# Performance work log

Hardware: AMD Instinct MI355X
Metric: run time of the kernel (lower is better)

Reference implementation:

```python
import jax, jax.numpy as jnp
import numpy as np

N = 20000      # total nodes (20 proteins x 1000 residues)
E = 320000     # edges (avg degree 16)
F_IN = 22      # amino-acid feature dim
H = 4          # attention heads
C = 64         # hidden dim per head
HC = H * C     # 256
G = 20         # number of graphs
OUT = 128      # output embedding dim
NEG_SLOPE = 0.2


def setup_inputs() -> dict:
    key = jax.random.key(0)
    ks = jax.random.split(key, 24)
    x = jax.random.normal(ks[0], (N, F_IN), dtype=jnp.float32)
    edge_index = jax.random.randint(ks[1], (2, E), 0, N)
    batch = jnp.arange(N, dtype=jnp.int64) // (N // G)  # 1000 nodes per graph
    s = 0.1
    d = {
        'x': x, 'edge_index': edge_index, 'batch': batch,
        'Win': jax.random.normal(ks[2], (F_IN, C)) * s,
        'bin_': jnp.zeros((C,), jnp.float32),
        'Wout': jax.random.normal(ks[3], (2 * HC, OUT)) * s,
        'bout': jnp.zeros((OUT,), jnp.float32),
    }
    kidx = 4
    for i in range(3):
        in_dim = C if i == 0 else HC
        d[f'Wl{i}'] = jax.random.normal(ks[kidx], (in_dim, HC)) * s; kidx += 1
        d[f'Wr{i}'] = jax.random.normal(ks[kidx], (in_dim, HC)) * s; kidx += 1
        d[f'att{i}'] = jax.random.normal(ks[kidx], (H, C)) * s; kidx += 1
        d[f'b{i}'] = jnp.zeros((HC,), jnp.float32)
    return d


def _gatv2_layer(h, src, dst, Wl, Wr, att, bias):
    # PyG GATv2Conv (share_weights=False, concat=True), dropout off (eval)
    xl = (h @ Wl).reshape(-1, H, C)   # source transform (x_j)
    xr = (h @ Wr).reshape(-1, H, C)   # target transform (x_i)
    e = jax.nn.leaky_relu(xl[src] + xr[dst], NEG_SLOPE)  # [E+N, H, C]
    logit = jnp.einsum('ehc,hc->eh', e, att)             # [E+N, H]
    mx = jax.ops.segment_max(logit, dst, num_segments=N)
    mx = jnp.where(jnp.isfinite(mx), mx, 0.0)
    ex = jnp.exp(logit - mx[dst])
    den = jax.ops.segment_sum(ex, dst, num_segments=N)
    alpha = ex / (den[dst] + 1e-16)                      # segment softmax
    out = jax.ops.segment_sum(alpha[:, :, None] * xl[src], dst, num_segments=N)
    return out.reshape(-1, HC) + bias


def reference(x, edge_index, batch, Win, bin_,
              Wl0, Wr0, att0, b0, Wl1, Wr1, att1, b1, Wl2, Wr2, att2, b2,
              Wout, bout):
    # add self-loops once (add_self_loops=True in every GATv2Conv)
    loops = jnp.arange(N, dtype=edge_index.dtype)
    src = jnp.concatenate([edge_index[0], loops])
    dst = jnp.concatenate([edge_index[1], loops])

    h = jax.nn.relu(x @ Win + bin_)  # input_proj + ReLU (dropout = eval identity)
    layers = [(Wl0, Wr0, att0, b0), (Wl1, Wr1, att1, b1), (Wl2, Wr2, att2, b2)]
    for (Wl, Wr, att, b) in layers:
        h_prev = h
        h = jax.nn.elu(_gatv2_layer(h, src, dst, Wl, Wr, att, b))
        if h_prev.shape[-1] == h.shape[-1]:  # residual when dims match (layers 1,2)
            h = h + h_prev

    counts = jax.ops.segment_sum(jnp.ones((N,), h.dtype), batch, num_segments=G)
    x_mean = jax.ops.segment_sum(h, batch, num_segments=G) / counts[:, None]
    x_max = jax.ops.segment_max(h, batch, num_segments=G)
    x_global = jnp.concatenate([x_mean, x_max], axis=-1)  # [G, 512]
    return x_global @ Wout + bout                          # [G, 128]
```

## Files before the change

kernel.cpp:

```cpp
#include <hip/hip_runtime.h>
#include <hip/hip_bf16.h>
#include <math.h>

#define N_NODES 20000
#define N_EDGES 320000
#define F_IN 22
#define H_HEADS 4
#define C_DIM 64
#define HC 256
#define G_GRAPHS 20
#define OUT_DIM 128
#define NODES_PER_G 1000
#define POOL_CHUNKS 8
#define NODES_PER_CHUNK (NODES_PER_G / POOL_CHUNKS)
#define ELL_CAP 64
#define SCAT_NB ((N_EDGES + 255) / 256)
#define INPROJ_NB (N_NODES / 4)

#if __has_builtin(__builtin_amdgcn_exp2f)
#define EXP2F __builtin_amdgcn_exp2f
#else
#define EXP2F exp2f
#endif

typedef unsigned short ushortT;
typedef __attribute__((ext_vector_type(8))) short short8;
typedef __attribute__((ext_vector_type(4))) float v4f;
typedef __attribute__((ext_vector_type(2))) float f2;

typedef const __attribute__((address_space(1))) void* gas_p;
typedef __attribute__((address_space(3))) void* las_p;

__device__ inline ushortT f2bf(float f) {
    unsigned int u = __float_as_uint(f);
    unsigned int r = (u + 0x7fffu + ((u >> 16) & 1u)) >> 16;
    return (ushortT)r;
}

__global__ __launch_bounds__(256) void front_kernel(
        const int* __restrict__ esrc, const int* __restrict__ edst,
        int* __restrict__ fill, int* __restrict__ ell,
        const float* __restrict__ x, const float* __restrict__ Win,
        const float* __restrict__ bin, ushortT* __restrict__ h0b,
        const float* __restrict__ Wl0, const float* __restrict__ Wr0,
        const float* __restrict__ Wl1, const float* __restrict__ Wr1,
        const float* __restrict__ Wl2, const float* __restrict__ Wr2,
        ushortT* __restrict__ Bt0, ushortT* __restrict__ Bt1, ushortT* __restrict__ Bt2) {
    int tid = threadIdx.x;
    if (blockIdx.x < SCAT_NB) {
        int i = blockIdx.x * 256 + tid;
        if (i < N_EDGES) {
            int d = edst[i];
            int p = atomicAdd(&fill[d], 1);
            if (p < ELL_CAP) ell[(d << 6) + p] = esrc[i];
        }
        return;
    }
    if (blockIdx.x < SCAT_NB + INPROJ_NB) {
        int node = (blockIdx.x - SCAT_NB) * 4 + (tid >> 6);
        int c = tid & 63;
        float acc = bin[c];
        const float* xr = x + node * F_IN;
#pragma unroll
        for (int f = 0; f < F_IN; f++) acc += xr[f] * Win[f * C_DIM + c];
        h0b[node * C_DIM + c] = f2bf(acc > 0.f ? acc : 0.f);
        return;
    }
    int flat = blockIdx.x - SCAT_NB - INPROJ_NB;
    int z = flat >> 6;
    int rem = flat & 63;
    int kx = (rem >> 3) * 32;
    int nx = (rem & 7) * 32;
    int layer = z >> 1, isR = z & 1;
    const float* src; ushortT* dst; int K;
    if (layer == 0)      { K = 64;  dst = Bt0; src = isR ? Wr0 : Wl0; }
    else if (layer == 1) { K = 256; dst = Bt1; src = isR ? Wr1 : Wl1; }
    else                 { K = 256; dst = Bt2; src = isR ? Wr2 : Wl2; }
    if (kx >= K) return;
    __shared__ float tile[32][33];
    int c = tid & 31, r8 = tid >> 5;
#pragma unroll
    for (int i = 0; i < 4; i++) {
        int kk = r8 + i * 8;
        tile[kk][c] = src[(kx + kk) * 256 + nx + c];
    }
    __syncthreads();
    int nbase = isR ? 256 : 0;
#pragma unroll
    for (int i = 0; i < 4; i++) {
        int nn = r8 + i * 8;
        dst[(size_t)(nbase + nx + nn) * K + kx + c] = f2bf(tile[c][nn]);
    }
}

#define GBM 128
#define GBN 128
#define GBK 32

__global__ __launch_bounds__(256) void gemm_mfma_kernel(
        const ushortT* __restrict__ A, const ushortT* __restrict__ Bt,
        ushortT* __restrict__ XLb, ushortT* __restrict__ XRb, int M, int K) {
    __shared__ ushortT As[GBM * GBK];
    __shared__ ushortT Bs[GBN * GBK];
    int tid = threadIdx.x;
    int wave = tid >> 6, lane = tid & 63;
    int wm = wave & 1, wn = wave >> 1;
    int bm0 = blockIdx.y * GBM;
    int bn0 = blockIdx.x * GBN;

    v4f acc[4][4];
#pragma unroll
    for (int mt = 0; mt < 4; mt++)
#pragma unroll
        for (int nt = 0; nt < 4; nt++) acc[mt][nt] = (v4f){0.f, 0.f, 0.f, 0.f};

    int srow = lane >> 2;
    int scol = (lane & 3) * 8;
    int arow0 = wave * 16 + srow;
    int arow1 = arow0 + 64;
    int ag0 = bm0 + arow0; if (ag0 >= M) ag0 = 0;
    int ag1 = bm0 + arow1; if (ag1 >= M) ag1 = 0;
    const ushortT* aptr0 = A + (size_t)ag0 * K + scol;
    const ushortT* aptr1 = A + (size_t)ag1 * K + scol;
    const ushortT* bptr0 = Bt + (size_t)(bn0 + arow0) * K + scol;
    const ushortT* bptr1 = Bt + (size_t)(bn0 + arow1) * K + scol;
    las_p lA0 = (las_p)&As[(wave * 16) * GBK];
    las_p lA1 = (las_p)&As[(wave * 16 + 64) * GBK];
    las_p lB0 = (las_p)&Bs[(wave * 16) * GBK];
    las_p lB1 = (las_p)&Bs[(wave * 16 + 64) * GBK];

    int mrow = lane & 15;
    int koff = (lane >> 4) * 8;

    for (int k0 = 0; k0 < K; k0 += GBK) {
        __builtin_amdgcn_global_load_lds((gas_p)(aptr0 + k0), lA0, 16, 0, 0);
        __builtin_amdgcn_global_load_lds((gas_p)(aptr1 + k0), lA1, 16, 0, 0);
        __builtin_amdgcn_global_load_lds((gas_p)(bptr0 + k0), lB0, 16, 0, 0);
        __builtin_amdgcn_global_load_lds((gas_p)(bptr1 + k0), lB1, 16, 0, 0);
        __syncthreads();
        short8 af[4], bf[4];
#pragma unroll
        for (int mt = 0; mt < 4; mt++)
            af[mt] = *(const short8*)&As[(wm * 64 + mt * 16 + mrow) * GBK + koff];
#pragma unroll
        for (int nt = 0; nt < 4; nt++)
            bf[nt] = *(const short8*)&Bs[(wn * 64 + nt * 16 + mrow) * GBK + koff];
#pragma unroll
        for (int mt = 0; mt < 4; mt++)
#pragma unroll
            for (int nt = 0; nt < 4; nt++)
                acc[mt][nt] = __builtin_amdgcn_mfma_f32_16x16x32_bf16(af[mt], bf[nt], acc[mt][nt], 0, 0, 0);
        __syncthreads();
    }

    int cbase = bn0 + wn * 64;
    ushortT* dst = XLb;
    if (cbase >= 256) { dst = XRb; cbase -= 256; }
    int col = cbase + (lane & 15);
    int rbase = bm0 + wm * 64 + ((lane >> 4) * 4);
#pragma unroll
    for (int mt = 0; mt < 4; mt++) {
#pragma unroll
        for (int reg = 0; reg < 4; reg++) {
            int row = rbase + mt * 16 + reg;
            if (row < M) {
#pragma unroll
                for (int nt = 0; nt < 4; nt++)
                    dst[(size_t)row * 256 + col + nt * 16] = f2bf(acc[mt][nt][reg]);
            }
        }
    }
}

template <int PAT>
__device__ inline float swz_add(float p) {
    return p + __int_as_float(__builtin_amdgcn_ds_swizzle(__float_as_int(p), PAT));
}

__device__ inline void gat_edge(uint2 curu, f2 xr01, f2 xr23, f2 at01, f2 at23,
                                float live, float& den, f2& acc01, f2& acc23) {
    f2 x01, x23;
    x01.x = __uint_as_float(curu.x << 16);
    x01.y = __uint_as_float(curu.x & 0xffff0000u);
    x23.x = __uint_as_float(curu.y << 16);
    x23.y = __uint_as_float(curu.y & 0xffff0000u);
    f2 t01 = x01 + xr01;
    f2 t23 = x23 + xr23;
    t01 = __builtin_elementwise_max(t01, t01 * 0.2f);
    t23 = __builtin_elementwise_max(t23, t23 * 0.2f);
    f2 pp = t01 * at01;
    pp = __builtin_elementwise_fma(t23, at23, pp);
    float p = pp.x + pp.y;
    p = swz_add<0x041F>(p);
    p = swz_add<0x081F>(p);
    p = swz_add<0x101F>(p);
    p = swz_add<0x201F>(p);
    p = fminf(p, 110.f);
    float w = EXP2F(p) * live;
    den += w;
    f2 wv = {w, w};
    acc01 = __builtin_elementwise_fma(wv, x01, acc01);
    acc23 = __builtin_elementwise_fma(wv, x23, acc23);
}

__global__ __launch_bounds__(256) void gat_layer_kernel(
        const ushortT* __restrict__ xlb, const ushortT* __restrict__ xrb,
        const int* __restrict__ ell, const int* __restrict__ fill,
        const float* __restrict__ att, const float* __restrict__ bias,
        const float* __restrict__ hprev,
        float* __restrict__ hout, ushortT* __restrict__ houtb) {
    int lane = threadIdx.x & 63;
    int d = blockIdx.x * 4 + (threadIdx.x >> 6);

    const uint2* xl2 = (const uint2*)xlb;
    uint2 xru = ((const uint2*)xrb)[d * 64 + lane];
    f2 xr01, xr23;
    xr01.x = __uint_as_float(xru.x << 16);
    xr01.y = __uint_as_float(xru.x & 0xffff0000u);
    xr23.x = __uint_as_float(xru.y << 16);
    xr23.y = __uint_as_float(xru.y & 0xffff0000u);

    float4 attv = ((const float4*)att)[lane];
    const float LOG2E = 1.44269504088896f;
    f2 at01 = {attv.x * LOG2E, attv.y * LOG2E};
    f2 at23 = {attv.z * LOG2E, attv.w * LOG2E};

    int deg = fill[d];
    if (deg > ELL_CAP - 1) deg = ELL_CAP - 1;
    int M = deg + 1;

    int idx = (lane < deg) ? ell[(d << 6) + lane] : d;

    float den = 0.f;
    f2 acc01 = {0.f, 0.f}, acc23 = {0.f, 0.f};

    uint2 buf[4];
#pragma unroll
    for (int k = 0; k < 4; k++) {
        int ni = __builtin_amdgcn_readlane(idx, k);
        buf[k] = xl2[(size_t)ni * 64 + lane];
    }
    int P = (M + 3) >> 2;
    for (int g = 0; g < P; g++) {
        int base = g * 4;
#pragma unroll
        for (int k = 0; k < 4; k++) {
            uint2 cur = buf[k];
            int ni = __builtin_amdgcn_readlane(idx, (base + 4 + k) & 63);
            buf[k] = xl2[(size_t)ni * 64 + lane];
            float live = (base + k < M) ? 1.0f : 0.0f;
            gat_edge(cur, xr01, xr23, at01, at23, live, den, acc01, acc23);
        }
    }

    float inv = 1.f / (den + 1e-16f);
    float4 bv = ((const float4*)bias)[lane];
    float4 v;
    v.x = acc01.x * inv + bv.x;
    v.y = acc01.y * inv + bv.y;
    v.z = acc23.x * inv + bv.z;
    v.w = acc23.y * inv + bv.w;
    v.x = v.x > 0.f ? v.x : __expf(v.x) - 1.f;
    v.y = v.y > 0.f ? v.y : __expf(v.y) - 1.f;
    v.z = v.z > 0.f ? v.z : __expf(v.z) - 1.f;
    v.w = v.w > 0.f ? v.w : __expf(v.w) - 1.f;
    if (hprev) {
        float4 hp = ((const float4*)hprev)[d * 64 + lane];
        v.x += hp.x; v.y += hp.y; v.z += hp.z; v.w += hp.w;
    }
    if (hout) ((float4*)hout)[d * 64 + lane] = v;
    uint2 pb;
    pb.x = (unsigned int)f2bf(v.x) | ((unsigned int)f2bf(v.y) << 16);
    pb.y = (unsigned int)f2bf(v.z) | ((unsigned int)f2bf(v.w) << 16);
    ((uint2*)houtb)[d * 64 + lane] = pb;
}

__global__ __launch_bounds__(256) void pool_partial_kernel(
        const ushortT* __restrict__ hb, float* __restrict__ psum, float* __restrict__ pmax) {
    int blk = blockIdx.x;
    int tid = threadIdx.x;
    int g = blk / POOL_CHUNKS;
    int ch = blk % POOL_CHUNKS;
    const ushortT* base = hb + ((size_t)g * NODES_PER_G + ch * NODES_PER_CHUNK) * HC;
    float sum = 0.f, mx = -INFINITY;
    for (int n = 0; n < NODES_PER_CHUNK; n++) {
        float v = __uint_as_float(((unsigned int)base[n * HC + tid]) << 16);
        sum += v;
        mx = fmaxf(mx, v);
    }
    psum[blk * HC + tid] = sum;
    pmax[blk * HC + tid] = mx;
}

__global__ __launch_bounds__(256) void pool_out_kernel(
        const float* __restrict__ psum, const float* __restrict__ pmax,
        const float* __restrict__ Wout, const float* __restrict__ bout,
        float* __restrict__ out) {
    int g = blockIdx.x;
    int tid = threadIdx.x;
    __shared__ float xg[2 * HC];
    float sum = 0.f, mx = -INFINITY;
    for (int c = 0; c < POOL_CHUNKS; c++) {
        sum += psum[(g * POOL_CHUNKS + c) * HC + tid];
        mx = fmaxf(mx, pmax[(g * POOL_CHUNKS + c) * HC + tid]);
    }
    xg[tid] = sum * (1.0f / NODES_PER_G);
    xg[HC + tid] = mx;
    __syncthreads();
    if (tid < OUT_DIM) {
        float acc = bout[tid];
        for (int j = 0; j < 2 * HC; j++) acc += xg[j] * Wout[j * OUT_DIM + tid];
        out[g * OUT_DIM + tid] = acc;
    }
}


extern "C" void kernel_launch(void* const* d_in, const int* in_sizes, int n_in,
                              void* d_out, int out_size, void* d_ws, size_t ws_size,
                              hipStream_t stream) {
    const float* x    = (const float*)d_in[0];
    const int*   ei   = (const int*)d_in[1];
    const float* Win  = (const float*)d_in[3];
    const float* bin  = (const float*)d_in[4];
    const float* Wout = (const float*)d_in[5];
    const float* bout = (const float*)d_in[6];
    const float* Wl[3] = {(const float*)d_in[7],  (const float*)d_in[11], (const float*)d_in[15]};
    const float* Wr[3] = {(const float*)d_in[8],  (const float*)d_in[12], (const float*)d_in[16]};
    const float* att[3] = {(const float*)d_in[9], (const float*)d_in[13], (const float*)d_in[17]};
    const float* bb[3] = {(const float*)d_in[10], (const float*)d_in[14], (const float*)d_in[18]};
    float* out = (float*)d_out;

    const int* esrc = ei;
    const int* edst = ei + N_EDGES;

    float* hA   = (float*)d_ws;
    float* hB   = hA + (size_t)N_NODES * HC;
    float* psum = hB + (size_t)N_NODES * HC;
    float* pmax = psum + (size_t)G_GRAPHS * POOL_CHUNKS * HC;
    ushortT* h0b = (ushortT*)(pmax + (size_t)G_GRAPHS * POOL_CHUNKS * HC);
    ushortT* hAb = h0b + (size_t)N_NODES * C_DIM;
    ushortT* hBb = hAb + (size_t)N_NODES * HC;
    ushortT* XLb = hBb + (size_t)N_NODES * HC;
    ushortT* XRb = XLb + (size_t)N_NODES * HC;
    ushortT* Bt0 = XRb + (size_t)N_NODES * HC;
    ushortT* Bt1 = Bt0 + 512 * 64;
    ushortT* Bt2 = Bt1 + 512 * 256;
    int* fill  = (int*)(Bt2 + 512 * 256);
    int* ell   = fill + N_NODES;

    (void)hipMemsetAsync(fill, 0, N_NODES * sizeof(int), stream);

    front_kernel<<<SCAT_NB + INPROJ_NB + 384, 256, 0, stream>>>(
        esrc, edst, fill, ell, x, Win, bin, h0b,
        Wl[0], Wr[0], Wl[1], Wr[1], Wl[2], Wr[2], Bt0, Bt1, Bt2);

    dim3 ggrid(512 / GBN, (N_NODES + GBM - 1) / GBM);

    gemm_mfma_kernel<<<ggrid, 256, 0, stream>>>(h0b, Bt0, XLb, XRb, N_NODES, C_DIM);
    gat_layer_kernel<<<N_NODES / 4, 256, 0, stream>>>(XLb, XRb, ell, fill, att[0], bb[0],
                                                      nullptr, hA, hAb);

    gemm_mfma_kernel<<<ggrid, 256, 0, stream>>>(hAb, Bt1, XLb, XRb, N_NODES, HC);
    gat_layer_kernel<<<N_NODES / 4, 256, 0, stream>>>(XLb, XRb, ell, fill, att[1], bb[1],
                                                      hA, hB, hBb);

    gemm_mfma_kernel<<<ggrid, 256, 0, stream>>>(hBb, Bt2, XLb, XRb, N_NODES, HC);
    gat_layer_kernel<<<N_NODES / 4, 256, 0, stream>>>(XLb, XRb, ell, fill, att[2], bb[2],
                                                      hB, nullptr, hAb);

    pool_partial_kernel<<<G_GRAPHS * POOL_CHUNKS, 256, 0, stream>>>(hAb, psum, pmax);
    pool_out_kernel<<<G_GRAPHS, 256, 0, stream>>>(psum, pmax, Wout, bout, out);
}
```

Before: 267.2 us.

## Fuse all stages into one cooperative persistent kernel with grid syncs

Replaces the chain of separate launches (front, three gemm+GAT pairs, two pooling kernels) with a single cooperative mega-kernel. Each stage runs its virtual blocks in a grid-stride loop, and grid.sync() separates the stages. This removes per-launch overhead and inter-kernel gaps. In exchange it adds grid-wide barriers, caps the grid at a number of resident blocks that may be below the old grid sizes, and can lose occupancy because register and LDS use is now the maximum across all fused stages.

```diff
diff --git a/kernel.cpp b/kernel.cpp
--- a/kernel.cpp
+++ b/kernel.cpp
@@ -1,6 +1,9 @@
 #include <hip/hip_runtime.h>
+#include <hip/hip_cooperative_groups.h>
 #include <hip/hip_bf16.h>
 #include <math.h>
+
+namespace cg = cooperative_groups;
 
 #define N_NODES 20000
 #define N_EDGES 320000
@@ -16,6 +19,10 @@
 #define ELL_CAP 64
 #define SCAT_NB ((N_EDGES + 255) / 256)
 #define INPROJ_NB (N_NODES / 4)
+#define FRONT_NV (SCAT_NB + INPROJ_NB + 384)
+#define GEMM_MT ((N_NODES + 127) / 128)
+#define GEMM_NV (4 * GEMM_MT)
+#define GAT_NV (N_NODES / 4)
 
 #if __has_builtin(__builtin_amdgcn_exp2f)
 #define EXP2F __builtin_amdgcn_exp2f
@@ -27,7 +34,6 @@
 typedef __attribute__((ext_vector_type(8))) short short8;
 typedef __attribute__((ext_vector_type(4))) float v4f;
 typedef __attribute__((ext_vector_type(2))) float f2;
-
 typedef const __attribute__((address_space(1))) void* gas_p;
 typedef __attribute__((address_space(3))) void* las_p;
 
@@ -37,47 +43,59 @@
     return (ushortT)r;
 }
 
-__global__ __launch_bounds__(256) void front_kernel(
-        const int* __restrict__ esrc, const int* __restrict__ edst,
-        int* __restrict__ fill, int* __restrict__ ell,
-        const float* __restrict__ x, const float* __restrict__ Win,
-        const float* __restrict__ bin, ushortT* __restrict__ h0b,
-        const float* __restrict__ Wl0, const float* __restrict__ Wr0,
-        const float* __restrict__ Wl1, const float* __restrict__ Wr1,
-        const float* __restrict__ Wl2, const float* __restrict__ Wr2,
-        ushortT* __restrict__ Bt0, ushortT* __restrict__ Bt1, ushortT* __restrict__ Bt2) {
-    int tid = threadIdx.x;
-    if (blockIdx.x < SCAT_NB) {
-        int i = blockIdx.x * 256 + tid;
+struct MegaArgs {
+    const int* esrc; const int* edst;
+    int* fill; int* ell;
+    const float* x; const float* Win; const float* bin;
+    ushortT* h0b;
+    const float* Wl0; const float* Wr0;
+    const float* Wl1; const float* Wr1;
+    const float* Wl2; const float* Wr2;
+    ushortT* Bt0; ushortT* Bt1; ushortT* Bt2;
+    const float* att0; const float* b0;
+    const float* att1; const float* b1;
+    const float* att2; const float* b2;
+    float* hA; float* hB;
+    ushortT* hAb; ushortT* hBb;
+    ushortT* XLb; ushortT* XRb;
+    float* psum; float* pmax;
+    const float* Wout; const float* bout;
+    float* out;
+};
+
+
+__device__ void front_body(int vb, int tid, const MegaArgs& a) {
+    if (vb < SCAT_NB) {
+        int i = vb * 256 + tid;
         if (i < N_EDGES) {
-            int d = edst[i];
-            int p = atomicAdd(&fill[d], 1);
-            if (p < ELL_CAP) ell[(d << 6) + p] = esrc[i];
+            int d = a.edst[i];
+            int p = atomicAdd(&a.fill[d], 1);
+            if (p < ELL_CAP) a.ell[(d << 6) + p] = a.esrc[i];
         }
         return;
     }
-    if (blockIdx.x < SCAT_NB + INPROJ_NB) {
-        int node = (blockIdx.x - SCAT_NB) * 4 + (tid >> 6);
+    if (vb < SCAT_NB + INPROJ_NB) {
+        int node = (vb - SCAT_NB) * 4 + (tid >> 6);
         int c = tid & 63;
-        float acc = bin[c];
-        const float* xr = x + node * F_IN;
-#pragma unroll
-        for (int f = 0; f < F_IN; f++) acc += xr[f] * Win[f * C_DIM + c];
-        h0b[node * C_DIM + c] = f2bf(acc > 0.f ? acc : 0.f);
+        float acc = a.bin[c];
+        const float* xr = a.x + node * F_IN;
+#pragma unroll
+        for (int f = 0; f < F_IN; f++) acc += xr[f] * a.Win[f * C_DIM + c];
+        a.h0b[node * C_DIM + c] = f2bf(acc > 0.f ? acc : 0.f);
         return;
     }
-    int flat = blockIdx.x - SCAT_NB - INPROJ_NB;
+    __shared__ float tile[32][33];
+    int flat = vb - SCAT_NB - INPROJ_NB;
     int z = flat >> 6;
     int rem = flat & 63;
     int kx = (rem >> 3) * 32;
     int nx = (rem & 7) * 32;
     int layer = z >> 1, isR = z & 1;
     const float* src; ushortT* dst; int K;
-    if (layer == 0)      { K = 64;  dst = Bt0; src = isR ? Wr0 : Wl0; }
-    else if (layer == 1) { K = 256; dst = Bt1; src = isR ? Wr1 : Wl1; }
-    else                 { K = 256; dst = Bt2; src = isR ? Wr2 : Wl2; }
+    if (layer == 0)      { K = 64;  dst = a.Bt0; src = isR ? a.Wr0 : a.Wl0; }
+    else if (layer == 1) { K = 256; dst = a.Bt1; src = isR ? a.Wr1 : a.Wl1; }
+    else                 { K = 256; dst = a.Bt2; src = isR ? a.Wr2 : a.Wl2; }
     if (kx >= K) return;
-    __shared__ float tile[32][33];
     int c = tid & 31, r8 = tid >> 5;
 #pragma unroll
     for (int i = 0; i < 4; i++) {
@@ -91,22 +109,21 @@
         int nn = r8 + i * 8;
         dst[(size_t)(nbase + nx + nn) * K + kx + c] = f2bf(tile[c][nn]);
     }
+    __syncthreads();
 }
 
 #define GBM 128
 #define GBN 128
 #define GBK 32
 
-__global__ __launch_bounds__(256) void gemm_mfma_kernel(
-        const ushortT* __restrict__ A, const ushortT* __restrict__ Bt,
-        ushortT* __restrict__ XLb, ushortT* __restrict__ XRb, int M, int K) {
+__device__ void gemm_body(int vb, int tid, const ushortT* A, const ushortT* Bt,
+                          ushortT* XLb, ushortT* XRb, int K) {
     __shared__ ushortT As[GBM * GBK];
     __shared__ ushortT Bs[GBN * GBK];
-    int tid = threadIdx.x;
     int wave = tid >> 6, lane = tid & 63;
     int wm = wave & 1, wn = wave >> 1;
-    int bm0 = blockIdx.y * GBM;
-    int bn0 = blockIdx.x * GBN;
+    int bn0 = (vb & 3) * GBN;
+    int bm0 = (vb >> 2) * GBM;
 
     v4f acc[4][4];
 #pragma unroll
@@ -118,8 +135,8 @@
     int scol = (lane & 3) * 8;
     int arow0 = wave * 16 + srow;
     int arow1 = arow0 + 64;
-    int ag0 = bm0 + arow0; if (ag0 >= M) ag0 = 0;
-    int ag1 = bm0 + arow1; if (ag1 >= M) ag1 = 0;
+    int ag0 = bm0 + arow0; if (ag0 >= N_NODES) ag0 = 0;
+    int ag1 = bm0 + arow1; if (ag1 >= N_NODES) ag1 = 0;
     const ushortT* aptr0 = A + (size_t)ag0 * K + scol;
     const ushortT* aptr1 = A + (size_t)ag1 * K + scol;
     const ushortT* bptr0 = Bt + (size_t)(bn0 + arow0) * K + scol;
@@ -163,7 +180,7 @@
 #pragma unroll
         for (int reg = 0; reg < 4; reg++) {
             int row = rbase + mt * 16 + reg;
-            if (row < M) {
+            if (row < N_NODES) {
 #pragma unroll
                 for (int nt = 0; nt < 4; nt++)
                     dst[(size_t)row * 256 + col + nt * 16] = f2bf(acc[mt][nt][reg]);
@@ -203,14 +220,13 @@
     acc23 = __builtin_elementwise_fma(wv, x23, acc23);
 }
 
-__global__ __launch_bounds__(256) void gat_layer_kernel(
-        const ushortT* __restrict__ xlb, const ushortT* __restrict__ xrb,
-        const int* __restrict__ ell, const int* __restrict__ fill,
-        const float* __restrict__ att, const float* __restrict__ bias,
-        const float* __restrict__ hprev,
-        float* __restrict__ hout, ushortT* __restrict__ houtb) {
-    int lane = threadIdx.x & 63;
-    int d = blockIdx.x * 4 + (threadIdx.x >> 6);
+__device__ void gat_body(int vb, int tid,
+                         const ushortT* xlb, const ushortT* xrb,
+                         const int* ell, const int* fill,
+                         const float* att, const float* bias,
+                         const float* hprev, float* hout, ushortT* houtb) {
+    int lane = tid & 63;
+    int d = vb * 4 + (tid >> 6);
 
     const uint2* xl2 = (const uint2*)xlb;
     uint2 xru = ((const uint2*)xrb)[d * 64 + lane];
@@ -275,12 +291,10 @@
     ((uint2*)houtb)[d * 64 + lane] = pb;
 }
 
-__global__ __launch_bounds__(256) void pool_partial_kernel(
-        const ushortT* __restrict__ hb, float* __restrict__ psum, float* __restrict__ pmax) {
-    int blk = blockIdx.x;
-    int tid = threadIdx.x;
-    int g = blk / POOL_CHUNKS;
-    int ch = blk % POOL_CHUNKS;
+__device__ void pool_partial_body(int vb, int tid, const ushortT* hb,
+                                  float* psum, float* pmax) {
+    int g = vb / POOL_CHUNKS;
+    int ch = vb % POOL_CHUNKS;
     const ushortT* base = hb + ((size_t)g * NODES_PER_G + ch * NODES_PER_CHUNK) * HC;
     float sum = 0.f, mx = -INFINITY;
     for (int n = 0; n < NODES_PER_CHUNK; n++) {
@@ -288,16 +302,12 @@
         sum += v;
         mx = fmaxf(mx, v);
     }
-    psum[blk * HC + tid] = sum;
-    pmax[blk * HC + tid] = mx;
-}
-
-__global__ __launch_bounds__(256) void pool_out_kernel(
-        const float* __restrict__ psum, const float* __restrict__ pmax,
-        const float* __restrict__ Wout, const float* __restrict__ bout,
-        float* __restrict__ out) {
-    int g = blockIdx.x;
-    int tid = threadIdx.x;
+    psum[vb * HC + tid] = sum;
+    pmax[vb * HC + tid] = mx;
+}
+
+__device__ void pool_out_body(int g, int tid, const float* psum, const float* pmax,
+                              const float* Wout, const float* bout, float* out) {
     __shared__ float xg[2 * HC];
     float sum = 0.f, mx = -INFINITY;
     for (int c = 0; c < POOL_CHUNKS; c++) {
@@ -312,6 +322,41 @@
         for (int j = 0; j < 2 * HC; j++) acc += xg[j] * Wout[j * OUT_DIM + tid];
         out[g * OUT_DIM + tid] = acc;
     }
+    __syncthreads();
+}
+
+__global__ __launch_bounds__(256, 4) void mega_kernel(MegaArgs a) {
+    cg::grid_group grid = cg::this_grid();
+    int tid = threadIdx.x;
+    int nb = gridDim.x;
+
+    for (int vb = blockIdx.x; vb < FRONT_NV; vb += nb) front_body(vb, tid, a);
+    grid.sync();
+
+    for (int layer = 0; layer < 3; layer++) {
+        const ushortT* A; const ushortT* Bt; int K;
+        if (layer == 0)      { A = a.h0b; Bt = a.Bt0; K = 64; }
+        else if (layer == 1) { A = a.hAb; Bt = a.Bt1; K = 256; }
+        else                 { A = a.hBb; Bt = a.Bt2; K = 256; }
+        for (int vb = blockIdx.x; vb < GEMM_NV; vb += nb)
+            gemm_body(vb, tid, A, Bt, a.XLb, a.XRb, K);
+        grid.sync();
+
+        const float* att; const float* bias; const float* hprev;
+        float* hout; ushortT* houtb;
+        if (layer == 0)      { att = a.att0; bias = a.b0; hprev = nullptr; hout = a.hA; houtb = a.hAb; }
+        else if (layer == 1) { att = a.att1; bias = a.b1; hprev = a.hA; hout = a.hB; houtb = a.hBb; }
+        else                 { att = a.att2; bias = a.b2; hprev = a.hB; hout = nullptr; houtb = a.hAb; }
+        for (int vb = blockIdx.x; vb < GAT_NV; vb += nb)
+            gat_body(vb, tid, a.XLb, a.XRb, a.ell, a.fill, att, bias, hprev, hout, houtb);
+        grid.sync();
+    }
+
+    for (int vb = blockIdx.x; vb < G_GRAPHS * POOL_CHUNKS; vb += nb)
+        pool_partial_body(vb, tid, a.hAb, a.psum, a.pmax);
+    grid.sync();
+    for (int vb = blockIdx.x; vb < G_GRAPHS; vb += nb)
+        pool_out_body(vb, tid, a.psum, a.pmax, a.Wout, a.bout, a.out);
 }
 
 
@@ -324,14 +369,6 @@
     const float* bin  = (const float*)d_in[4];
     const float* Wout = (const float*)d_in[5];
     const float* bout = (const float*)d_in[6];
-    const float* Wl[3] = {(const float*)d_in[7],  (const float*)d_in[11], (const float*)d_in[15]};
-    const float* Wr[3] = {(const float*)d_in[8],  (const float*)d_in[12], (const float*)d_in[16]};
-    const float* att[3] = {(const float*)d_in[9], (const float*)d_in[13], (const float*)d_in[17]};
-    const float* bb[3] = {(const float*)d_in[10], (const float*)d_in[14], (const float*)d_in[18]};
-    float* out = (float*)d_out;
-
-    const int* esrc = ei;
-    const int* edst = ei + N_EDGES;
 
     float* hA   = (float*)d_ws;
     float* hB   = hA + (size_t)N_NODES * HC;
@@ -350,24 +387,31 @@
 
     (void)hipMemsetAsync(fill, 0, N_NODES * sizeof(int), stream);
 
-    front_kernel<<<SCAT_NB + INPROJ_NB + 384, 256, 0, stream>>>(
-        esrc, edst, fill, ell, x, Win, bin, h0b,
-        Wl[0], Wr[0], Wl[1], Wr[1], Wl[2], Wr[2], Bt0, Bt1, Bt2);
-
-    dim3 ggrid(512 / GBN, (N_NODES + GBM - 1) / GBM);
-
-    gemm_mfma_kernel<<<ggrid, 256, 0, stream>>>(h0b, Bt0, XLb, XRb, N_NODES, C_DIM);
-    gat_layer_kernel<<<N_NODES / 4, 256, 0, stream>>>(XLb, XRb, ell, fill, att[0], bb[0],
-                                                      nullptr, hA, hAb);
-
-    gemm_mfma_kernel<<<ggrid, 256, 0, stream>>>(hAb, Bt1, XLb, XRb, N_NODES, HC);
-    gat_layer_kernel<<<N_NODES / 4, 256, 0, stream>>>(XLb, XRb, ell, fill, att[1], bb[1],
-                                                      hA, hB, hBb);
-
-    gemm_mfma_kernel<<<ggrid, 256, 0, stream>>>(hBb, Bt2, XLb, XRb, N_NODES, HC);
-    gat_layer_kernel<<<N_NODES / 4, 256, 0, stream>>>(XLb, XRb, ell, fill, att[2], bb[2],
-                                                      hB, nullptr, hAb);
-
-    pool_partial_kernel<<<G_GRAPHS * POOL_CHUNKS, 256, 0, stream>>>(hAb, psum, pmax);
-    pool_out_kernel<<<G_GRAPHS, 256, 0, stream>>>(psum, pmax, Wout, bout, out);
-}
+    MegaArgs ma;
+    ma.esrc = ei; ma.edst = ei + N_EDGES;
+    ma.fill = fill; ma.ell = ell;
+    ma.x = x; ma.Win = Win; ma.bin = bin; ma.h0b = h0b;
+    ma.Wl0 = (const float*)d_in[7];  ma.Wr0 = (const float*)d_in[8];
+    ma.att0 = (const float*)d_in[9]; ma.b0 = (const float*)d_in[10];
+    ma.Wl1 = (const float*)d_in[11]; ma.Wr1 = (const float*)d_in[12];
+    ma.att1 = (const float*)d_in[13]; ma.b1 = (const float*)d_in[14];
+    ma.Wl2 = (const float*)d_in[15]; ma.Wr2 = (const float*)d_in[16];
+    ma.att2 = (const float*)d_in[17]; ma.b2 = (const float*)d_in[18];
+    ma.Bt0 = Bt0; ma.Bt1 = Bt1; ma.Bt2 = Bt2;
+    ma.hA = hA; ma.hB = hB;
+    ma.hAb = hAb; ma.hBb = hBb;
+    ma.XLb = XLb; ma.XRb = XRb;
+    ma.psum = psum; ma.pmax = pmax;
+    ma.Wout = Wout; ma.bout = bout;
+    ma.out = (float*)d_out;
+
+    int maxb = 0;
+    (void)hipOccupancyMaxActiveBlocksPerMultiprocessor(&maxb, mega_kernel, 256, 0);
+    if (maxb < 1) maxb = 1;
+    int nb = maxb * 256;
+    if (nb > 1024) nb = 1024;
+
+    void* kargs[] = {&ma};
+    (void)hipLaunchCooperativeKernel((void*)mega_kernel, dim3(nb), dim3(256),
+                                     kargs, 0, stream);
+}
```

Result: slower. 841.2 us (+214.8%).

## Reorganize GEMM LDS tile layout and fuse pooling stages via last-block counter

Applied to the files above, without the earlier changes.

The GEMM's global-to-LDS staging now stores each 16-row slab as k-chunk-major groups, so the MFMA fragment reads hit consecutive LDS addresses and cause fewer bank conflicts. The two pooling kernels are merged into one: each block writes its partial sums, bumps an atomic counter, and the last block finishes all graphs' mean/max and the output projection. This saves a kernel launch, but the final projection for all 20 graphs now runs serially in a single block.

```diff
diff --git a/kernel.cpp b/kernel.cpp
--- a/kernel.cpp
+++ b/kernel.cpp
@@ -13,6 +13,7 @@
 #define NODES_PER_G 1000
 #define POOL_CHUNKS 8
 #define NODES_PER_CHUNK (NODES_PER_G / POOL_CHUNKS)
+#define POOL_NB (G_GRAPHS * POOL_CHUNKS)
 #define ELL_CAP 64
 #define SCAT_NB ((N_EDGES + 255) / 256)
 #define INPROJ_NB (N_NODES / 4)
@@ -27,7 +28,6 @@
 typedef __attribute__((ext_vector_type(8))) short short8;
 typedef __attribute__((ext_vector_type(4))) float v4f;
 typedef __attribute__((ext_vector_type(2))) float f2;
-
 typedef const __attribute__((address_space(1))) void* gas_p;
 typedef __attribute__((address_space(3))) void* las_p;
 
@@ -114,8 +114,8 @@
 #pragma unroll
         for (int nt = 0; nt < 4; nt++) acc[mt][nt] = (v4f){0.f, 0.f, 0.f, 0.f};
 
-    int srow = lane >> 2;
-    int scol = (lane & 3) * 8;
+    int srow = lane & 15;
+    int scol = (lane >> 4) * 8;
     int arow0 = wave * 16 + srow;
     int arow1 = arow0 + 64;
     int ag0 = bm0 + arow0; if (ag0 >= M) ag0 = 0;
@@ -124,13 +124,13 @@
     const ushortT* aptr1 = A + (size_t)ag1 * K + scol;
     const ushortT* bptr0 = Bt + (size_t)(bn0 + arow0) * K + scol;
     const ushortT* bptr1 = Bt + (size_t)(bn0 + arow1) * K + scol;
-    las_p lA0 = (las_p)&As[(wave * 16) * GBK];
-    las_p lA1 = (las_p)&As[(wave * 16 + 64) * GBK];
-    las_p lB0 = (las_p)&Bs[(wave * 16) * GBK];
-    las_p lB1 = (las_p)&Bs[(wave * 16 + 64) * GBK];
+    las_p lA0 = (las_p)&As[wave * 512];
+    las_p lA1 = (las_p)&As[(wave + 4) * 512];
+    las_p lB0 = (las_p)&Bs[wave * 512];
+    las_p lB1 = (las_p)&Bs[(wave + 4) * 512];
 
     int mrow = lane & 15;
-    int koff = (lane >> 4) * 8;
+    int kc = lane >> 4;
 
     for (int k0 = 0; k0 < K; k0 += GBK) {
         __builtin_amdgcn_global_load_lds((gas_p)(aptr0 + k0), lA0, 16, 0, 0);
@@ -140,11 +140,15 @@
         __syncthreads();
         short8 af[4], bf[4];
 #pragma unroll
-        for (int mt = 0; mt < 4; mt++)
-            af[mt] = *(const short8*)&As[(wm * 64 + mt * 16 + mrow) * GBK + koff];
-#pragma unroll
-        for (int nt = 0; nt < 4; nt++)
-            bf[nt] = *(const short8*)&Bs[(wn * 64 + nt * 16 + mrow) * GBK + koff];
+        for (int mt = 0; mt < 4; mt++) {
+            int s = wm * 4 + mt;
+            af[mt] = *(const short8*)&As[s * 512 + (kc * 16 + mrow) * 8];
+        }
+#pragma unroll
+        for (int nt = 0; nt < 4; nt++) {
+            int s = wn * 4 + nt;
+            bf[nt] = *(const short8*)&Bs[s * 512 + (kc * 16 + mrow) * 8];
+        }
 #pragma unroll
         for (int mt = 0; mt < 4; mt++)
 #pragma unroll
@@ -275,8 +279,10 @@
     ((uint2*)houtb)[d * 64 + lane] = pb;
 }
 
-__global__ __launch_bounds__(256) void pool_partial_kernel(
-        const ushortT* __restrict__ hb, float* __restrict__ psum, float* __restrict__ pmax) {
+__global__ __launch_bounds__(256) void pool_kernel(
+        const ushortT* __restrict__ hb, float* __restrict__ psum, float* __restrict__ pmax,
+        int* __restrict__ counter, const float* __restrict__ Wout,
+        const float* __restrict__ bout, float* __restrict__ out) {
     int blk = blockIdx.x;
     int tid = threadIdx.x;
     int g = blk / POOL_CHUNKS;
@@ -290,27 +296,30 @@
     }
     psum[blk * HC + tid] = sum;
     pmax[blk * HC + tid] = mx;
-}
-
-__global__ __launch_bounds__(256) void pool_out_kernel(
-        const float* __restrict__ psum, const float* __restrict__ pmax,
-        const float* __restrict__ Wout, const float* __restrict__ bout,
-        float* __restrict__ out) {
-    int g = blockIdx.x;
-    int tid = threadIdx.x;
+
+    __threadfence();
+    __shared__ int last;
+    __syncthreads();
+    if (tid == 0) last = (atomicAdd(counter, 1) == POOL_NB - 1) ? 1 : 0;
+    __syncthreads();
+    if (!last) return;
+
     __shared__ float xg[2 * HC];
-    float sum = 0.f, mx = -INFINITY;
-    for (int c = 0; c < POOL_CHUNKS; c++) {
-        sum += psum[(g * POOL_CHUNKS + c) * HC + tid];
-        mx = fmaxf(mx, pmax[(g * POOL_CHUNKS + c) * HC + tid]);
-    }
-    xg[tid] = sum * (1.0f / NODES_PER_G);
-    xg[HC + tid] = mx;
-    __syncthreads();
-    if (tid < OUT_DIM) {
-        float acc = bout[tid];
-        for (int j = 0; j < 2 * HC; j++) acc += xg[j] * Wout[j * OUT_DIM + tid];
-        out[g * OUT_DIM + tid] = acc;
+    for (int gg = 0; gg < G_GRAPHS; gg++) {
+        float s2 = 0.f, m2 = -INFINITY;
+        for (int c = 0; c < POOL_CHUNKS; c++) {
+            s2 += psum[(gg * POOL_CHUNKS + c) * HC + tid];
+            m2 = fmaxf(m2, pmax[(gg * POOL_CHUNKS + c) * HC + tid]);
+        }
+        xg[tid] = s2 * (1.0f / NODES_PER_G);
+        xg[HC + tid] = m2;
+        __syncthreads();
+        if (tid < OUT_DIM) {
+            float acc = bout[tid];
+            for (int j = 0; j < 2 * HC; j++) acc += xg[j] * Wout[j * OUT_DIM + tid];
+            out[gg * OUT_DIM + tid] = acc;
+        }
+        __syncthreads();
     }
 }
 
@@ -336,8 +345,8 @@
     float* hA   = (float*)d_ws;
     float* hB   = hA + (size_t)N_NODES * HC;
     float* psum = hB + (size_t)N_NODES * HC;
-    float* pmax = psum + (size_t)G_GRAPHS * POOL_CHUNKS * HC;
-    ushortT* h0b = (ushortT*)(pmax + (size_t)G_GRAPHS * POOL_CHUNKS * HC);
+    float* pmax = psum + (size_t)POOL_NB * HC;
+    ushortT* h0b = (ushortT*)(pmax + (size_t)POOL_NB * HC);
     ushortT* hAb = h0b + (size_t)N_NODES * C_DIM;
     ushortT* hBb = hAb + (size_t)N_NODES * HC;
     ushortT* XLb = hBb + (size_t)N_NODES * HC;
@@ -346,9 +355,10 @@
     ushortT* Bt1 = Bt0 + 512 * 64;
     ushortT* Bt2 = Bt1 + 512 * 256;
     int* fill  = (int*)(Bt2 + 512 * 256);
-    int* ell   = fill + N_NODES;
-
-    (void)hipMemsetAsync(fill, 0, N_NODES * sizeof(int), stream);
+    int* counter = fill + N_NODES;
+    int* ell   = counter + 1;
+
+    (void)hipMemsetAsync(fill, 0, (N_NODES + 1) * sizeof(int), stream);
 
     front_kernel<<<SCAT_NB + INPROJ_NB + 384, 256, 0, stream>>>(
         esrc, edst, fill, ell, x, Win, bin, h0b,
@@ -368,6 +378,5 @@
     gat_layer_kernel<<<N_NODES / 4, 256, 0, stream>>>(XLb, XRb, ell, fill, att[2], bb[2],
                                                       hB, nullptr, hAb);
 
-    pool_partial_kernel<<<G_GRAPHS * POOL_CHUNKS, 256, 0, stream>>>(hAb, psum, pmax);
-    pool_out_kernel<<<G_GRAPHS, 256, 0, stream>>>(psum, pmax, Wout, bout, out);
-}
+    pool_kernel<<<POOL_NB, 256, 0, stream>>>(hAb, psum, pmax, counter, Wout, bout, out);
+}
```

Result: slower. 394.4 us (+47.6%).
